# Kernel tuning notes

Measured on AMD Instinct MI355X. Metric: run time of the kernel, lower is better.

The kernel has to match this reference:

```python
import jax, jax.numpy as jnp
import numpy as np


def _oct_table():
    # e_i * e_j = sgn[i,j] * e_{idx[i,j]}  (standard Fano-plane octonion table)
    idx = np.zeros((8, 8), dtype=np.int32)
    sgn = np.zeros((8, 8), dtype=np.float32)
    for j in range(8):
        idx[0, j] = j; sgn[0, j] = 1.0
    for i in range(1, 8):
        idx[i, 0] = i; sgn[i, 0] = 1.0
        idx[i, i] = 0; sgn[i, i] = -1.0
    for (a, b, c) in [(1, 2, 3), (1, 4, 5), (1, 7, 6), (2, 4, 6), (2, 5, 7), (3, 4, 7), (3, 6, 5)]:
        for (p, q, r) in ((a, b, c), (b, c, a), (c, a, b)):
            idx[p, q] = r; sgn[p, q] = 1.0
            idx[q, p] = r; sgn[q, p] = -1.0
    # For output part k and weight part i, J[k,i] is the unique input part j
    # with e_i*e_j = SG[k,i]*e_k.
    J = np.zeros((8, 8), dtype=np.int32)
    SG = np.zeros((8, 8), dtype=np.float32)
    for i in range(8):
        for j in range(8):
            k = idx[i, j]
            J[k, i] = j; SG[k, i] = sgn[i, j]
    return J, SG

_J, _SG = _oct_table()
_SGj = jnp.asarray(_SG)


def ternary_quant(W):
    # BitNet-style: per-matrix abs-mean scale, round+clip to {-1,0,1}, rescale.
    scale = jnp.mean(jnp.abs(W), axis=(1, 2), keepdims=True)
    return jnp.clip(jnp.round(W / (scale + 1e-8)), -1.0, 1.0) * scale


def oct_linear(x, W):
    # x: [B,T,Cin] (8 concatenated parts), W: [8, Pout, Pin]
    B, T, Cin = x.shape
    xp = x.reshape(B, T, 8, Cin // 8)
    Wq = ternary_quant(W)
    outs = []
    for k in range(8):  # fixed structural loop over octonion components
        xm = _SGj[k][None, None, :, None] * xp[:, :, _J[k], :]  # [B,T,8,Pin]
        outs.append(jnp.einsum('btip,iop->bto', xm, Wq))
    return jnp.concatenate(outs, axis=-1)  # [B,T,8*Pout]


def rmsnorm(x, w, eps=1e-6):
    return x * jax.lax.rsqrt(jnp.mean(x * x, axis=-1, keepdims=True) + eps) * w


def rope(x, cos, sin):
    # x: [B,T,H,D] with complex pairs (even, odd); cos/sin: [T,D/2]
    xr, xi = x[..., 0::2], x[..., 1::2]
    c = cos[None, :, None, :]
    s = sin[None, :, None, :]
    out_r = xr * c - xi * s
    out_i = xr * s + xi * c
    return jnp.stack([out_r, out_i], axis=-1).reshape(x.shape)


def setup_inputs() -> dict:
    B, T, C, H = 4, 1024, 2048, 16
    HD = C // H            # 128
    HIDDEN = 5464          # ceil(int(2*4*C/3)/8)*8
    key = jax.random.key(0)
    ks = jax.random.split(key, 10)
    x = jax.random.normal(ks[0], (B, T, C), jnp.float32)
    theta = 10000.0
    freqs = 1.0 / (theta ** (np.arange(0, HD, 2, dtype=np.float32) / HD))
    ang = np.arange(T, dtype=np.float32)[:, None] * freqs[None, :]
    w = lambda k, shape: jax.random.normal(k, shape, jnp.float32) * 0.02
    return {
        'x': x,
        'freqs_cos': jnp.asarray(np.cos(ang), jnp.float32),
        'freqs_sin': jnp.asarray(np.sin(ang), jnp.float32),
        'attn_norm_w': jnp.ones((C,), jnp.float32),
        'ffn_norm_w': jnp.ones((C,), jnp.float32),
        'wq': w(ks[1], (8, C // 8, C // 8)),
        'wk': w(ks[2], (8, C // 8, C // 8)),
        'wv': w(ks[3], (8, C // 8, C // 8)),
        'wo': w(ks[4], (8, C // 8, C // 8)),
        'w_gate': w(ks[5], (8, HIDDEN // 8, C // 8)),
        'w_up': w(ks[6], (8, HIDDEN // 8, C // 8)),
        'w_down': w(ks[7], (8, C // 8, HIDDEN // 8)),
    }


def reference(x, freqs_cos, freqs_sin, attn_norm_w, ffn_norm_w,
              wq, wk, wv, wo, w_gate, w_up, w_down):
    B, T, C = x.shape
    H = 16
    HD = C // H
    # attention sub-block
    xn = rmsnorm(x, attn_norm_w)
    q = oct_linear(xn, wq).reshape(B, T, H, HD)
    k = oct_linear(xn, wk).reshape(B, T, H, HD)
    v = oct_linear(xn, wv).reshape(B, T, H, HD)
    q = rope(q, freqs_cos, freqs_sin)
    k = rope(k, freqs_cos, freqs_sin)
    q, k, v = (t.transpose(0, 2, 1, 3) for t in (q, k, v))  # [B,H,T,D]
    scores = jnp.einsum('bhqd,bhkd->bhqk', q, k) / jnp.sqrt(jnp.float32(HD))
    causal = jnp.tril(jnp.ones((T, T), dtype=bool))
    scores = jnp.where(causal[None, None], scores, jnp.float32(-1e30))
    att = jax.nn.softmax(scores, axis=-1)
    y = jnp.einsum('bhqk,bhkd->bhqd', att, v).transpose(0, 2, 1, 3).reshape(B, T, C)
    h = x + oct_linear(y, wo)
    # SwiGLU MLP sub-block
    hn = rmsnorm(h, ffn_norm_w)
    gate = oct_linear(hn, w_gate)
    up = oct_linear(hn, w_up)
    ff = oct_linear(jax.nn.silu(gate) * up, w_down)
    return h + ff
```

## Files before the change

kernel.cpp:

```cpp
#include <hip/hip_runtime.h>
#include <stdint.h>

typedef __bf16 bf16;
typedef __bf16 bf16x8 __attribute__((ext_vector_type(8)));
typedef float f32x4 __attribute__((ext_vector_type(4)));

typedef const uint32_t __attribute__((address_space(1))) guint_t;
typedef uint32_t __attribute__((address_space(3))) luint_t;

__device__ __forceinline__ void gload_lds16(const void* g, void* l) {
  __builtin_amdgcn_global_load_lds((guint_t*)g, (luint_t*)l, 16, 0, 0);
}

struct OctTab { int J[64]; float SG[64]; };
struct Ptr7 { const float* p[7]; int opsz[7]; };

__global__ __launch_bounds__(256) void scales_kernel(Ptr7 t, float* __restrict__ scales) {
  int bx = blockIdx.x;
  int ti = bx >> 3, i = bx & 7;
  int n = t.opsz[ti];
  const float4* base = (const float4*)(t.p[ti] + (size_t)i * n);
  int n4 = n >> 2;
  float s = 0.f;
  for (int j = threadIdx.x; j < n4; j += 256) {
    float4 v = base[j];
    s += fabsf(v.x) + fabsf(v.y) + fabsf(v.z) + fabsf(v.w);
  }
#pragma unroll
  for (int off = 32; off >= 1; off >>= 1) s += __shfl_xor(s, off);
  __shared__ float red[4];
  int lane = threadIdx.x & 63, wvi = threadIdx.x >> 6;
  if (lane == 0) red[wvi] = s;
  __syncthreads();
  if (threadIdx.x == 0) scales[bx] = (red[0] + red[1] + red[2] + red[3]) / (float)n;
}

__global__ __launch_bounds__(256) void build_dense_kernel(
    const float* __restrict__ W, const float* __restrict__ scales,
    bf16* __restrict__ Wt, int O, int P, int ld, int rowOff, int total, OctTab tab) {
  int idx = blockIdx.x * 256 + threadIdx.x;
  if (idx >= total) return;
  int p = idx % P;
  int rest = idx / P;
  int o = rest % O;
  rest /= O;
  int i = rest & 7;
  int k = rest >> 3;
  float s = scales[i];
  float w = W[((size_t)i * O + o) * P + p];
  float q = rintf(w / (s + 1e-8f));
  q = fminf(1.f, fmaxf(-1.f, q)) * s;
  int j = tab.J[k * 8 + i];
  float sg = tab.SG[k * 8 + i];
  Wt[(size_t)(rowOff + k * O + o) * ld + j * P + p] = (bf16)(sg * q);
}

__global__ __launch_bounds__(256) void zero_pad_kernel(bf16* __restrict__ Wd) {
  int idx = blockIdx.x * 256 + threadIdx.x;
  if (idx >= 81920) return;
  int row = idx / 40, c = idx % 40;
  Wd[(size_t)row * 5504 + 5464 + c] = (bf16)0.f;
}

__global__ __launch_bounds__(256) void rmsnorm_kernel(
    const float* __restrict__ x, const float* __restrict__ w, bf16* __restrict__ out) {
  int row = blockIdx.x;
  int tid = threadIdx.x;
  const float4* xp = (const float4*)(x + (size_t)row * 2048);
  float4 a = xp[tid * 2], b = xp[tid * 2 + 1];
  float ss = a.x*a.x + a.y*a.y + a.z*a.z + a.w*a.w
           + b.x*b.x + b.y*b.y + b.z*b.z + b.w*b.w;
#pragma unroll
  for (int off = 32; off >= 1; off >>= 1) ss += __shfl_xor(ss, off);
  __shared__ float red[4];
  int lane = tid & 63, wvi = tid >> 6;
  if (lane == 0) red[wvi] = ss;
  __syncthreads();
  float tot = red[0] + red[1] + red[2] + red[3];
  float rms = rsqrtf(tot * (1.f / 2048.f) + 1e-6f);
  const float4* wp = (const float4*)w;
  float4 wa = wp[tid * 2], wb = wp[tid * 2 + 1];
  bf16x8 ov;
  ov[0] = (bf16)(a.x * rms * wa.x); ov[1] = (bf16)(a.y * rms * wa.y);
  ov[2] = (bf16)(a.z * rms * wa.z); ov[3] = (bf16)(a.w * rms * wa.w);
  ov[4] = (bf16)(b.x * rms * wb.x); ov[5] = (bf16)(b.y * rms * wb.y);
  ov[6] = (bf16)(b.z * rms * wb.z); ov[7] = (bf16)(b.w * rms * wb.w);
  *(bf16x8*)(out + (size_t)row * 2048 + tid * 8) = ov;
}

template <int MODE>
__global__ __launch_bounds__(256) void gemm_bt(
    const bf16* __restrict__ A, const bf16* __restrict__ Bt,
    const float* __restrict__ res, void* __restrict__ Cout, int N, int K) {
  __shared__ char smem[32768];
  char* As = smem;
  char* Bs = smem + 16384;
  int tid = threadIdx.x;
  int lane = tid & 63, wave = tid >> 6;
  int bm = blockIdx.y * 128, bn = blockIdx.x * 128;
  int wr = (wave >> 1) * 64, wc = (wave & 1) * 64;
  int r = lane & 15, g = lane >> 4;
  int srow = lane >> 3, scp = lane & 7;
  f32x4 acc[4][4] = {};
  for (int k0 = 0; k0 < K; k0 += 64) {
#pragma unroll
    for (int c = 0; c < 4; ++c) {
      int chunk = wave * 4 + c;
      int row = chunk * 8 + srow;
      int sc = ((scp ^ (row & 7)) << 3);
      gload_lds16(A + (size_t)(bm + row) * K + k0 + sc, As + chunk * 1024);
      gload_lds16(Bt + (size_t)(bn + row) * K + k0 + sc, Bs + chunk * 1024);
    }
    asm volatile("s_waitcnt vmcnt(0)" ::: "memory");
    __syncthreads();
#pragma unroll
    for (int kk = 0; kk < 2; ++kk) {
      bf16x8 af[4], bfv[4];
#pragma unroll
      for (int m = 0; m < 4; ++m) {
        int rowm = wr + m * 16 + r;
        int cc = (kk * 4 + g) ^ (rowm & 7);
        af[m] = *(const bf16x8*)(As + rowm * 128 + cc * 16);
      }
#pragma unroll
      for (int n = 0; n < 4; ++n) {
        int rown = wc + n * 16 + r;
        int cc = (kk * 4 + g) ^ (rown & 7);
        bfv[n] = *(const bf16x8*)(Bs + rown * 128 + cc * 16);
      }
#pragma unroll
      for (int m = 0; m < 4; ++m)
#pragma unroll
        for (int n = 0; n < 4; ++n)
          acc[m][n] = __builtin_amdgcn_mfma_f32_16x16x32_bf16(af[m], bfv[n], acc[m][n], 0, 0, 0);
    }
    __syncthreads();
  }
#pragma unroll
  for (int m = 0; m < 4; ++m) {
    int row0 = bm + wr + m * 16 + g * 4;
#pragma unroll
    for (int n = 0; n < 4; ++n) {
      int col = bn + wc + n * 16 + r;
#pragma unroll
      for (int j = 0; j < 4; ++j) {
        size_t off = (size_t)(row0 + j) * N + col;
        if (MODE == 0) ((bf16*)Cout)[off] = (bf16)acc[m][n][j];
        else           ((float*)Cout)[off] = acc[m][n][j] + res[off];
      }
    }
  }
}

__global__ __launch_bounds__(256) void rope_kernel(
    bf16* __restrict__ qkv, const float* __restrict__ fc, const float* __restrict__ fs) {
  int tid = blockIdx.x * 256 + threadIdx.x;
  int ub = tid & 15;
  int h = (tid >> 4) & 15;
  int qk = (tid >> 8) & 1;
  int row = tid >> 9;
  int t = row & 1023;
  bf16* p = qkv + (size_t)row * 6144 + qk * 2048 + h * 128 + ub * 8;
  bf16x8 v = *(bf16x8*)p;
  const float4 cv = *(const float4*)(fc + t * 64 + ub * 4);
  const float4 sv = *(const float4*)(fs + t * 64 + ub * 4);
  float cr[4] = {cv.x, cv.y, cv.z, cv.w};
  float sr[4] = {sv.x, sv.y, sv.z, sv.w};
  bf16x8 ov;
#pragma unroll
  for (int u = 0; u < 4; ++u) {
    float xr = (float)v[2 * u], xi = (float)v[2 * u + 1];
    ov[2 * u]     = (bf16)(xr * cr[u] - xi * sr[u]);
    ov[2 * u + 1] = (bf16)(xr * sr[u] + xi * cr[u]);
  }
  *(bf16x8*)p = ov;
}

__global__ __launch_bounds__(256) void attn_kernel(
    const bf16* __restrict__ qkv, bf16* __restrict__ y) {
  __shared__ bf16 Vt[128][40];
  __shared__ bf16 P[4][16][40];
  int tid = threadIdx.x;
  int lane = tid & 63, wvi = tid >> 6;
  int bh = blockIdx.x, qt = blockIdx.y;
  int b = bh >> 4, h = bh & 15;
  int q0 = qt * 64;
  int r = lane & 15, g = lane >> 4;
  const bf16* base = qkv + (size_t)b * 1024 * 6144;
  bf16x8 qf[4];
  {
    const bf16* qp = base + (size_t)(q0 + wvi * 16 + r) * 6144 + h * 128 + g * 8;
#pragma unroll
    for (int kk = 0; kk < 4; ++kk) qf[kk] = *(const bf16x8*)(qp + kk * 32);
  }
  f32x4 o[8];
#pragma unroll
  for (int d = 0; d < 8; ++d) o[d] = (f32x4){0.f, 0.f, 0.f, 0.f};
  float m_run[4], l_run[4];
#pragma unroll
  for (int j = 0; j < 4; ++j) { m_run[j] = -1e30f; l_run[j] = 0.f; }
  const float sc = 0.08838834764831845f;
  int nch = (q0 >> 5) + 2;
  for (int c = 0; c < nch; ++c) {
    __syncthreads();
#pragma unroll
    for (int it = 0; it < 2; ++it) {
      int e = it * 256 + tid;
      int vr = e >> 4, dg = e & 15;
      bf16x8 vvv = *(const bf16x8*)(base + (size_t)(c * 32 + vr) * 6144 + 4096 + h * 128 + dg * 8);
#pragma unroll
      for (int u = 0; u < 8; ++u) Vt[dg * 8 + u][vr] = vvv[u];
    }
    __syncthreads();
    f32x4 s0 = {0, 0, 0, 0}, s1 = {0, 0, 0, 0};
    const bf16* kp = base + (size_t)(c * 32 + r) * 6144 + 2048 + h * 128 + g * 8;
#pragma unroll
    for (int kk = 0; kk < 4; ++kk) {
      bf16x8 kf0 = *(const bf16x8*)(kp + kk * 32);
      bf16x8 kf1 = *(const bf16x8*)(kp + (size_t)16 * 6144 + kk * 32);
      s0 = __builtin_amdgcn_mfma_f32_16x16x32_bf16(qf[kk], kf0, s0, 0, 0, 0);
      s1 = __builtin_amdgcn_mfma_f32_16x16x32_bf16(qf[kk], kf1, s1, 0, 0, 0);
    }
    int qrow = q0 + wvi * 16 + g * 4;
    int kc = c * 32 + r;
    float pmax[4];
#pragma unroll
    for (int j = 0; j < 4; ++j) {
      float a0 = s0[j] * sc, a1 = s1[j] * sc;
      if (kc > qrow + j) a0 = -1e30f;
      if (kc + 16 > qrow + j) a1 = -1e30f;
      s0[j] = a0; s1[j] = a1;
      pmax[j] = fmaxf(a0, a1);
    }
#pragma unroll
    for (int j = 0; j < 4; ++j) {
#pragma unroll
      for (int w = 8; w >= 1; w >>= 1) pmax[j] = fmaxf(pmax[j], __shfl_xor(pmax[j], w));
    }
    float corr[4], rsum[4];
#pragma unroll
    for (int j = 0; j < 4; ++j) {
      float nm = fmaxf(m_run[j], pmax[j]);
      corr[j] = __expf(m_run[j] - nm);
      m_run[j] = nm;
      float p0 = __expf(s0[j] - nm), p1 = __expf(s1[j] - nm);
      s0[j] = p0; s1[j] = p1;
      rsum[j] = p0 + p1;
    }
#pragma unroll
    for (int j = 0; j < 4; ++j) {
#pragma unroll
      for (int w = 8; w >= 1; w >>= 1) rsum[j] += __shfl_xor(rsum[j], w);
      l_run[j] = l_run[j] * corr[j] + rsum[j];
      P[wvi][g * 4 + j][r] = (bf16)s0[j];
      P[wvi][g * 4 + j][16 + r] = (bf16)s1[j];
    }
#pragma unroll
    for (int d = 0; d < 8; ++d)
#pragma unroll
      for (int j = 0; j < 4; ++j) o[d][j] *= corr[j];
    asm volatile("s_waitcnt lgkmcnt(0)" ::: "memory");
    bf16x8 pa = *(const bf16x8*)&P[wvi][r][g * 8];
#pragma unroll
    for (int d = 0; d < 8; ++d) {
      bf16x8 vb = *(const bf16x8*)&Vt[d * 16 + r][g * 8];
      o[d] = __builtin_amdgcn_mfma_f32_16x16x32_bf16(pa, vb, o[d], 0, 0, 0);
    }
  }
#pragma unroll
  for (int j = 0; j < 4; ++j) {
    float inv = 1.f / l_run[j];
    size_t row = (size_t)(b * 1024 + q0 + wvi * 16 + g * 4 + j);
    bf16* yp = y + row * 2048 + h * 128 + r;
#pragma unroll
    for (int d = 0; d < 8; ++d) yp[d * 16] = (bf16)(o[d][j] * inv);
  }
}

__global__ __launch_bounds__(256) void silu_kernel(
    const bf16* __restrict__ up, bf16* __restrict__ gate_act) {
  int tid = blockIdx.x * 256 + threadIdx.x;
  int jb = tid % 688;
  int row = tid / 688;
  size_t off = (size_t)row * 5504 + jb * 8;
  bf16x8 ov;
  if (jb < 683) {
    bf16x8 gv = *(const bf16x8*)(gate_act + off);
    bf16x8 uv = *(const bf16x8*)(up + off);
#pragma unroll
    for (int u = 0; u < 8; ++u) {
      float gg = (float)gv[u], uu = (float)uv[u];
      ov[u] = (bf16)(gg / (1.f + __expf(-gg)) * uu);
    }
  } else {
#pragma unroll
    for (int u = 0; u < 8; ++u) ov[u] = (bf16)0.f;
  }
  *(bf16x8*)(gate_act + off) = ov;
}

static void build_oct(OctTab& t) {
  int idx[8][8]; float sgn[8][8];
  for (int j = 0; j < 8; ++j) { idx[0][j] = j; sgn[0][j] = 1.f; }
  for (int i = 1; i < 8; ++i) {
    idx[i][0] = i; sgn[i][0] = 1.f;
    idx[i][i] = 0; sgn[i][i] = -1.f;
  }
  const int tr[7][3] = {{1,2,3},{1,4,5},{1,7,6},{2,4,6},{2,5,7},{3,4,7},{3,6,5}};
  for (int ti = 0; ti < 7; ++ti) {
    int a = tr[ti][0], b = tr[ti][1], c = tr[ti][2];
    int cyc[3][3] = {{a,b,c},{b,c,a},{c,a,b}};
    for (int ci = 0; ci < 3; ++ci) {
      int p = cyc[ci][0], q = cyc[ci][1], r = cyc[ci][2];
      idx[p][q] = r; sgn[p][q] = 1.f;
      idx[q][p] = r; sgn[q][p] = -1.f;
    }
  }
  for (int i = 0; i < 8; ++i)
    for (int j = 0; j < 8; ++j) {
      int k = idx[i][j];
      t.J[k * 8 + i] = j;
      t.SG[k * 8 + i] = sgn[i][j];
    }
}

#define OFF_SCALES 0ull
#define OFF_WBUF   256ull
#define OFF_R16    (OFF_WBUF + 25165824ull)
#define OFF_QKVR   (OFF_R16 + 16777216ull)
#define OFF_H      (OFF_QKVR + 50331648ull)
#define OFF_G1     (OFF_H + 33554432ull)
#define WS_NEED    (OFF_G1 + 45088768ull)

extern "C" void kernel_launch(void* const* d_in, const int* in_sizes, int n_in,
                              void* d_out, int out_size, void* d_ws, size_t ws_size,
                              hipStream_t stream) {
  (void)in_sizes; (void)n_in; (void)out_size;
  if (ws_size < WS_NEED) return;

  const float* x   = (const float*)d_in[0];
  const float* fc  = (const float*)d_in[1];
  const float* fs  = (const float*)d_in[2];
  const float* anw = (const float*)d_in[3];
  const float* fnw = (const float*)d_in[4];
  const float* wqw = (const float*)d_in[5];
  const float* wkw = (const float*)d_in[6];
  const float* wvw = (const float*)d_in[7];
  const float* wow = (const float*)d_in[8];
  const float* wgw = (const float*)d_in[9];
  const float* wuw = (const float*)d_in[10];
  const float* wdw = (const float*)d_in[11];

  char* ws = (char*)d_ws;
  float* scales = (float*)(ws + OFF_SCALES);
  bf16* Wbuf = (bf16*)(ws + OFF_WBUF);
  bf16* xn   = (bf16*)(ws + OFF_R16);
  bf16* qkv  = (bf16*)(ws + OFF_QKVR);
  float* h   = (float*)(ws + OFF_H);
  bf16* g1   = (bf16*)(ws + OFF_G1);

  OctTab tab; build_oct(tab);
  Ptr7 p7;
  p7.p[0] = wqw; p7.p[1] = wkw; p7.p[2] = wvw; p7.p[3] = wow;
  p7.p[4] = wgw; p7.p[5] = wuw; p7.p[6] = wdw;
  for (int i = 0; i < 4; ++i) p7.opsz[i] = 65536;
  for (int i = 4; i < 7; ++i) p7.opsz[i] = 174848;

  scales_kernel<<<56, 256, 0, stream>>>(p7, scales);

  build_dense_kernel<<<16384, 256, 0, stream>>>(wqw, scales + 0,  Wbuf, 256, 256, 2048, 0,    4194304, tab);
  build_dense_kernel<<<16384, 256, 0, stream>>>(wkw, scales + 8,  Wbuf, 256, 256, 2048, 2048, 4194304, tab);
  build_dense_kernel<<<16384, 256, 0, stream>>>(wvw, scales + 16, Wbuf, 256, 256, 2048, 4096, 4194304, tab);
  rmsnorm_kernel<<<4096, 256, 0, stream>>>(x, anw, xn);
  gemm_bt<0><<<dim3(48, 32), 256, 0, stream>>>(xn, Wbuf, nullptr, qkv, 6144, 2048);
  rope_kernel<<<8192, 256, 0, stream>>>(qkv, fc, fs);
  attn_kernel<<<dim3(64, 16), 256, 0, stream>>>(qkv, (bf16*)(ws + OFF_R16) );

  build_dense_kernel<<<16384, 256, 0, stream>>>(wow, scales + 24, Wbuf, 256, 256, 2048, 0, 4194304, tab);
  gemm_bt<1><<<dim3(16, 32), 256, 0, stream>>>((bf16*)(ws + OFF_R16), Wbuf, x, h, 2048, 2048);

  bf16* hn = (bf16*)(ws + OFF_R16);
  rmsnorm_kernel<<<4096, 256, 0, stream>>>(h, fnw, hn);
  build_dense_kernel<<<43712, 256, 0, stream>>>(wgw, scales + 32, Wbuf, 683, 256, 2048, 0, 11190272, tab);
  gemm_bt<0><<<dim3(43, 32), 256, 0, stream>>>(hn, Wbuf, nullptr, g1, 5504, 2048);
  bf16* up = (bf16*)(ws + OFF_QKVR);
  build_dense_kernel<<<43712, 256, 0, stream>>>(wuw, scales + 40, Wbuf, 683, 256, 2048, 0, 11190272, tab);
  gemm_bt<0><<<dim3(43, 32), 256, 0, stream>>>(hn, Wbuf, nullptr, up, 5504, 2048);
  silu_kernel<<<11008, 256, 0, stream>>>(up, g1);
  build_dense_kernel<<<43712, 256, 0, stream>>>(wdw, scales + 48, Wbuf, 256, 683, 5504, 0, 11190272, tab);
  zero_pad_kernel<<<320, 256, 0, stream>>>(Wbuf);
  gemm_bt<1><<<dim3(16, 32), 256, 0, stream>>>(g1, Wbuf, h, (float*)d_out, 2048, 5504);
}
```

Baseline: 1.056 ms.

## Add double-buffered 256x256 GEMM, XCD-aware tile remap, and swizzled attention V tile

Adds a 512-thread GEMM kernel with 256x256 output tiles and double-buffered direct-to-LDS loads, which issues the next K-slice before computing the current one. It also raises MFMA wave priority during compute. This kernel replaces the 128x128 GEMM for the QKV, gate and up projections, to get more data reuse per tile and to hide load latency. Both GEMMs now remap block indices so that neighbouring tiles land on the same XCD, for better L2 locality. The attention kernel XOR-swizzles the transposed V tile in LDS to reduce bank conflicts. The trade-offs are 128KB of LDS per block, which limits occupancy, and wider tiles that read Bt rows past N on the padded grids.

New measurement: 989.7 us. 6.3% less time.

```diff
diff --git a/kernel.cpp b/kernel.cpp
--- a/kernel.cpp
+++ b/kernel.cpp
@@ -97,7 +97,10 @@
   char* Bs = smem + 16384;
   int tid = threadIdx.x;
   int lane = tid & 63, wave = tid >> 6;
-  int bm = blockIdx.y * 128, bn = blockIdx.x * 128;
+  int nwg = gridDim.x * gridDim.y;
+  int lin = blockIdx.y * gridDim.x + blockIdx.x;
+  if ((nwg & 7) == 0) lin = (lin & 7) * (nwg >> 3) + (lin >> 3);
+  int bm = (lin / gridDim.x) * 128, bn = (lin % gridDim.x) * 128;
   int wr = (wave >> 1) * 64, wc = (wave & 1) * 64;
   int r = lane & 15, g = lane >> 4;
   int srow = lane >> 3, scp = lane & 7;
@@ -147,6 +150,107 @@
         size_t off = (size_t)(row0 + j) * N + col;
         if (MODE == 0) ((bf16*)Cout)[off] = (bf16)acc[m][n][j];
         else           ((float*)Cout)[off] = acc[m][n][j] + res[off];
+      }
+    }
+  }
+}
+
+template <int MODE>
+__global__ __launch_bounds__(512, 2) void gemm256(
+    const bf16* __restrict__ A, const bf16* __restrict__ Bt,
+    const float* __restrict__ res, void* __restrict__ Cout,
+    int K, int Nst, int ldC) {
+  __shared__ char smem[131072];
+  const int tid = threadIdx.x;
+  const int lane = tid & 63, wave = tid >> 6;
+  int nwg = gridDim.x * gridDim.y;
+  int lin = blockIdx.y * gridDim.x + blockIdx.x;
+  if ((nwg & 7) == 0) lin = (lin & 7) * (nwg >> 3) + (lin >> 3);
+  const int bm = (lin / gridDim.x) * 256;
+  const int bn = (lin % gridDim.x) * 256;
+  const int wm = wave >> 2, wn = wave & 3;
+  const int r = lane & 15, g = lane >> 4;
+  const int srow = lane >> 3, sslot = lane & 7;
+  const int stg_row = wave * 32 + srow;
+
+  f32x4 acc[8][4] = {};
+  const int nkt = K >> 6;
+
+  auto STAGE = [&](int kt, int buf) {
+    char* ab = smem + buf * 32768;
+    char* bb = smem + 65536 + buf * 32768;
+    int k0 = kt << 6;
+#pragma unroll
+    for (int c = 0; c < 4; ++c) {
+      int row = stg_row + c * 8;
+      int sc = ((sslot ^ (row & 7)) << 3);
+      gload_lds16(A + (size_t)(bm + row) * K + k0 + sc, ab + (wave * 4 + c) * 1024);
+      gload_lds16(Bt + (size_t)(bn + row) * K + k0 + sc, bb + (wave * 4 + c) * 1024);
+    }
+  };
+
+  STAGE(0, 0);
+  int cur = 0;
+  for (int kt = 0; kt < nkt; ++kt) {
+    if (kt + 1 < nkt) {
+      STAGE(kt + 1, cur ^ 1);
+      asm volatile("s_waitcnt vmcnt(8)" ::: "memory");
+    } else {
+      asm volatile("s_waitcnt vmcnt(0)" ::: "memory");
+    }
+    __builtin_amdgcn_s_barrier();
+    const char* ab = smem + cur * 32768;
+    const char* bb = smem + 65536 + cur * 32768;
+    bf16x8 bfr[4][2];
+#pragma unroll
+    for (int p = 0; p < 4; ++p) {
+      if (p == 0) {
+#pragma unroll
+        for (int n = 0; n < 4; ++n)
+#pragma unroll
+          for (int kk = 0; kk < 2; ++kk) {
+            int rown = wn * 64 + n * 16 + r;
+            int cc = (kk * 4 + g) ^ (rown & 7);
+            bfr[n][kk] = *(const bf16x8*)(bb + rown * 128 + cc * 16);
+          }
+      }
+      bf16x8 af[2][2];
+#pragma unroll
+      for (int q = 0; q < 2; ++q)
+#pragma unroll
+        for (int kk = 0; kk < 2; ++kk) {
+          int rowm = wm * 128 + p * 32 + q * 16 + r;
+          int cc = (kk * 4 + g) ^ (rowm & 7);
+          af[q][kk] = *(const bf16x8*)(ab + rowm * 128 + cc * 16);
+        }
+      __builtin_amdgcn_s_barrier();
+      __builtin_amdgcn_s_setprio(1);
+#pragma unroll
+      for (int q = 0; q < 2; ++q)
+#pragma unroll
+        for (int n = 0; n < 4; ++n)
+#pragma unroll
+          for (int kk = 0; kk < 2; ++kk)
+            acc[p * 2 + q][n] = __builtin_amdgcn_mfma_f32_16x16x32_bf16(
+                af[q][kk], bfr[n][kk], acc[p * 2 + q][n], 0, 0, 0);
+      __builtin_amdgcn_s_setprio(0);
+      __builtin_amdgcn_s_barrier();
+    }
+    cur ^= 1;
+  }
+#pragma unroll
+  for (int mf = 0; mf < 8; ++mf) {
+    int row0 = bm + wm * 128 + mf * 16 + g * 4;
+#pragma unroll
+    for (int nf = 0; nf < 4; ++nf) {
+      int col = bn + wn * 64 + nf * 16 + r;
+      if (col < Nst) {
+#pragma unroll
+        for (int j = 0; j < 4; ++j) {
+          size_t off = (size_t)(row0 + j) * ldC + col;
+          if (MODE == 0) ((bf16*)Cout)[off] = (bf16)acc[mf][nf][j];
+          else           ((float*)Cout)[off] = acc[mf][nf][j] + res[off];
+        }
       }
     }
   }
@@ -208,8 +312,12 @@
       int e = it * 256 + tid;
       int vr = e >> 4, dg = e & 15;
       bf16x8 vvv = *(const bf16x8*)(base + (size_t)(c * 32 + vr) * 6144 + 4096 + h * 128 + dg * 8);
-#pragma unroll
-      for (int u = 0; u < 8; ++u) Vt[dg * 8 + u][vr] = vvv[u];
+      int ub = vr >> 3, uo = vr & 7;
+#pragma unroll
+      for (int u = 0; u < 8; ++u) {
+        int R = dg * 8 + u;
+        Vt[R][((ub ^ ((R >> 3) & 3)) << 3) + uo] = vvv[u];
+      }
     }
     __syncthreads();
     f32x4 s0 = {0, 0, 0, 0}, s1 = {0, 0, 0, 0};
@@ -263,7 +371,8 @@
     bf16x8 pa = *(const bf16x8*)&P[wvi][r][g * 8];
 #pragma unroll
     for (int d = 0; d < 8; ++d) {
-      bf16x8 vb = *(const bf16x8*)&Vt[d * 16 + r][g * 8];
+      int R = d * 16 + r;
+      bf16x8 vb = *(const bf16x8*)&Vt[R][(g ^ ((R >> 3) & 3)) << 3];
       o[d] = __builtin_amdgcn_mfma_f32_16x16x32_bf16(pa, vb, o[d], 0, 0, 0);
     }
   }
@@ -372,7 +481,7 @@
   build_dense_kernel<<<16384, 256, 0, stream>>>(wkw, scales + 8,  Wbuf, 256, 256, 2048, 2048, 4194304, tab);
   build_dense_kernel<<<16384, 256, 0, stream>>>(wvw, scales + 16, Wbuf, 256, 256, 2048, 4096, 4194304, tab);
   rmsnorm_kernel<<<4096, 256, 0, stream>>>(x, anw, xn);
-  gemm_bt<0><<<dim3(48, 32), 256, 0, stream>>>(xn, Wbuf, nullptr, qkv, 6144, 2048);
+  gemm256<0><<<dim3(24, 16), 512, 0, stream>>>(xn, Wbuf, nullptr, qkv, 2048, 6144, 6144);
   rope_kernel<<<8192, 256, 0, stream>>>(qkv, fc, fs);
   attn_kernel<<<dim3(64, 16), 256, 0, stream>>>(qkv, (bf16*)(ws + OFF_R16) );
 
@@ -382,10 +491,10 @@
   bf16* hn = (bf16*)(ws + OFF_R16);
   rmsnorm_kernel<<<4096, 256, 0, stream>>>(h, fnw, hn);
   build_dense_kernel<<<43712, 256, 0, stream>>>(wgw, scales + 32, Wbuf, 683, 256, 2048, 0, 11190272, tab);
-  gemm_bt<0><<<dim3(43, 32), 256, 0, stream>>>(hn, Wbuf, nullptr, g1, 5504, 2048);
+  gemm256<0><<<dim3(22, 16), 512, 0, stream>>>(hn, Wbuf, nullptr, g1, 2048, 5504, 5504);
   bf16* up = (bf16*)(ws + OFF_QKVR);
   build_dense_kernel<<<43712, 256, 0, stream>>>(wuw, scales + 40, Wbuf, 683, 256, 2048, 0, 11190272, tab);
-  gemm_bt<0><<<dim3(43, 32), 256, 0, stream>>>(hn, Wbuf, nullptr, up, 5504, 2048);
+  gemm256<0><<<dim3(22, 16), 512, 0, stream>>>(hn, Wbuf, nullptr, up, 2048, 5504, 5504);
   silu_kernel<<<11008, 256, 0, stream>>>(up, g1);
   build_dense_kernel<<<43712, 256, 0, stream>>>(wdw, scales + 48, Wbuf, 256, 683, 5504, 0, 11190272, tab);
   zero_pad_kernel<<<320, 256, 0, stream>>>(Wbuf);
```
